# Kernel optimization log

Measured on AMD Instinct MI355X. Metric: run time of the kernel, lower is better.

## Reference

```python
import jax, jax.numpy as jnp
import numpy as np
from math import factorial

H = W = 1024
NSC = 4   # n_scales
NOR = 4   # n_orientations
NA = 9


def _grids(h, w):
    # normalized frequency grids, DC at (h//2, w//2) after fftshift
    x = (jnp.arange(w) - w // 2) / (w / 2)
    y = (jnp.arange(h) - h // 2) / (h / 2)
    xr, yr = jnp.meshgrid(x, y, indexing='xy')  # (h, w)
    ang = jnp.arctan2(yr, xr)
    rad = jnp.sqrt(xr * xr + yr * yr)
    rad = rad.at[h // 2, w // 2].set(rad[h // 2, w // 2 - 1])  # avoid log2(0)
    return jnp.log2(rad), ang


def _rc(lr, shift):
    # raised-cosine transition of width 1 (in log2 radius); returns (hi, lo) masks
    t = jnp.clip(lr + shift, 0.0, 1.0)
    return jnp.sin(0.5 * jnp.pi * t), jnp.cos(0.5 * jnp.pi * t)


def _build_pyr(im):
    """Complex steerable pyramid in the frequency domain (downsampled),
    returning (residual highpass, oriented complex bands, residual lowpass,
    unoriented bandpass per scale)."""
    h, w = im.shape
    lr, _ = _grids(h, w)
    hi0m, lo0m = _rc(lr, 1.0)
    imdft = jnp.fft.fftshift(jnp.fft.fft2(im))
    hi0 = jnp.fft.ifft2(jnp.fft.ifftshift(imdft * hi0m)).real
    lodft = imdft * lo0m
    order = NOR - 1
    const = (2.0 ** (2 * order)) * (factorial(order) ** 2) / (NOR * factorial(2 * order))
    bands, unor = [], []
    for s in range(NSC):
        hh, ww = lodft.shape
        lr, ang = _grids(hh, ww)
        him, _ = _rc(lr, 2.0)
        for b in range(NOR):
            th = ang - jnp.pi * b / NOR
            thw = jnp.mod(th + jnp.pi, 2.0 * jnp.pi) - jnp.pi
            am = 2.0 * np.sqrt(const) * (jnp.cos(th) ** order) * (jnp.abs(thw) < jnp.pi / 2)
            bdft = ((-1j) ** order) * lodft * (am * him)
            bands.append(jnp.fft.ifft2(jnp.fft.ifftshift(bdft)))
        unor.append(jnp.fft.ifft2(jnp.fft.ifftshift(lodft * him)).real)
        # downsample lowpass by 2 (crop center of spectrum), apply next lo mask
        lodft = lodft[hh // 4: hh - hh // 4, ww // 4: ww - ww // 4]
        lr2, _ = _grids(hh // 2, ww // 2)
        _, lom = _rc(lr2, 1.0)
        lodft = lodft * lom
    lowpass = jnp.fft.ifft2(jnp.fft.ifftshift(lodft)).real
    return hi0, bands, lowpass, unor


def _autocorr_crop(x, denom, le):
    F = jnp.fft.fft2(x)
    ac = jnp.fft.fftshift(jnp.fft.ifft2(F * jnp.conj(F)).real) / denom
    cx, cy = x.shape[0] // 2, x.shape[1] // 2
    return ac[cx - le: cx + le + 1, cy - le: cy + le + 1]


def _expand(t, f):
    # frequency-domain upsampling by factor f (zero-pad centered spectrum)
    mx, my = t.shape
    T = (f * f) * jnp.fft.fftshift(jnp.fft.fft2(t))
    Te = jnp.zeros((f * mx, f * my), dtype=T.dtype)
    cx, cy = f * mx // 2, f * my // 2
    Te = Te.at[cx - mx // 2: cx + mx // 2, cy - my // 2: cy + my // 2].set(T)
    return jnp.fft.ifft2(jnp.fft.ifftshift(Te))


def _ps_stats(im0):
    S, O, Na = NSC, NOR, NA
    n = im0.size
    mn0, mx0 = jnp.min(im0), jnp.max(im0)
    mean0 = jnp.mean(im0)
    var0 = jnp.sum((im0 - mean0) ** 2) / (n - 1)  # unbiased, like torch.var
    skew0 = jnp.mean((im0 - mean0) ** 3) / var0 ** 1.5
    kurt0 = jnp.mean(jnp.abs(im0 - mean0) ** 4) / var0 ** 2
    statg0 = jnp.stack([mean0, var0, skew0, kurt0, mn0, mx0])

    hi0, bands, lowpass, unor = _build_pyr(im0)
    lowpass = lowpass - jnp.mean(lowpass)
    pyr = [hi0] + bands + [lowpass]
    apyr = [jnp.abs(c) for c in pyr]
    magMeans = jnp.stack([jnp.mean(a) for a in apyr])
    apyr = [a - magMeans[i] for i, a in enumerate(apyr)]

    la = (Na - 1) // 2
    acr = jnp.zeros((Na, Na, S + 1), jnp.float32)
    ace = jnp.zeros((Na, Na, S, O), jnp.float32)
    skew0p = jnp.zeros((S + 1,), jnp.float32)
    kurt0p = jnp.zeros((S + 1,), jnp.float32)

    # ---- lowpass residual: re-filter with height-0 pyramid lowpass (lo0 mask) ----
    ch = lowpass
    le = min(min(ch.shape) // 2 - 1, la)
    lr, _ = _grids(ch.shape[0], ch.shape[1])
    _, lo0m = _rc(lr, 1.0)
    imlp = jnp.fft.ifft2(jnp.fft.ifftshift(jnp.fft.fftshift(jnp.fft.fft2(ch)) * lo0m)).real
    ac = _autocorr_crop(imlp, ch.size, le)
    acr = acr.at[la - le: la + le + 1, la - le: la + le + 1, S].set(ac)
    vari = ac[le, le]
    ok = vari / var0 > 1e-6
    skew0p = skew0p.at[S].set(jnp.where(ok, jnp.mean(imlp ** 3) / vari ** 1.5, 0.0))
    kurt0p = kurt0p.at[S].set(jnp.where(ok, jnp.mean(imlp ** 4) / vari ** 2, 3.0))

    # ---- per-band magnitude autocorr + unoriented band moments ----
    for s in range(S):
        le = la
        for b in range(O):
            chb = apyr[s * O + b + 1]
            le = min(min(chb.shape) // 2 - 1, la)
            ac = _autocorr_crop(chb, chb.size, le)
            ace = ace.at[la - le: la + le + 1, la - le: la + le + 1, s, b].set(ac)
        chu = unor[s]
        # torch stacks (real, zeros): numel doubles, cubic/quartic means halve
        ac = _autocorr_crop(chu, 2 * chu.size, le)
        acr = acr.at[la - le: la + le + 1, la - le: la + le + 1, s].set(ac)
        vari = ac[le, le]
        ok = vari / var0 > 1e-6
        skew0p = skew0p.at[s].set(jnp.where(ok, 0.5 * jnp.mean(chu ** 3) / vari ** 1.5, 0.0))
        kurt0p = kurt0p.at[s].set(jnp.where(ok, 0.5 * jnp.mean(chu ** 4) / vari ** 2, 3.0))

    # ---- cross-orientation / cross-scale correlations ----
    C0 = jnp.zeros((O, O, S + 1), jnp.float32)
    Cx0 = jnp.zeros((O, O, S), jnp.float32)
    Cr0 = jnp.zeros((2 * O, 2 * O, S + 1), jnp.float32)
    Crx0 = jnp.zeros((2 * O, 2 * O, S), jnp.float32)
    for s in range(S):
        csz = pyr[s * O + 1].size
        if s < S - 1:
            pc, rc = [], []
            for b in range(O):
                tmp = _expand(pyr[(s + 1) * O + b + 1], 2) / 4
                r, i = tmp.real, tmp.imag
                mag = jnp.sqrt(r * r + i * i)
                ph = 2.0 * jnp.arctan2(r, i)  # swapped args: faithful to source
                rc.append((mag * jnp.cos(ph), mag * jnp.sin(ph)))
                pc.append(mag)  # |(rt2, it2)| == mag
            parents = jnp.stack([(m - m.mean()).T.ravel() for m in pc], 1)
            rparents = jnp.stack([r.T.ravel() for r, _ in rc] + [i.T.ravel() for _, i in rc], 1)
        else:
            tmp = _expand(lowpass, 2).real / 4
            rparents = jnp.stack([
                tmp.ravel(),
                jnp.roll(tmp, (0, 1), (0, 1)).ravel(),
                jnp.roll(tmp, (0, -1), (0, 1)).ravel(),
                jnp.roll(tmp, (1, 0), (0, 1)).ravel(),
                jnp.roll(tmp, (-1, 0), (0, 1)).ravel()], 1)
            parents = None
        cous = jnp.stack([apyr[s * O + b + 1].T.ravel() for b in range(O)], 1)
        C0 = C0.at[:, :, s].set(cous.T @ cous / csz)
        if parents is not None:
            Cx0 = Cx0.at[:, :, s].set(cous.T @ parents / csz)
        rcous = jnp.stack([pyr[s * O + b + 1].real.T.ravel() for b in range(O)], 1)
        Cr0 = Cr0.at[:O, :O, s].set(rcous.T @ rcous / csz)
        nrp = rparents.shape[1]
        Crx0 = Crx0.at[:O, :nrp, s].set(rcous.T @ rparents / csz)
        if s == S - 1:
            Cr0 = Cr0.at[:nrp, :nrp, S].set(rparents.T @ rparents / (csz / 4))

    vHPR0 = jnp.mean(hi0 ** 2)
    return jnp.concatenate([
        statg0, magMeans, ace.ravel(), skew0p, kurt0p, acr.ravel(),
        C0.ravel(), Cx0.ravel(), Cr0.ravel(), Crx0.ravel(), vHPR0[None]])


def setup_inputs() -> dict:
    key = jax.random.key(0)
    im0 = jax.random.normal(key, (H, W), dtype=jnp.float32)
    return {"im0": im0}


def reference(im0):
    return _ps_stats(im0)
```

## Files before the change

### kernel.cpp

```cpp
#include <hip/hip_runtime.h>

#define PI_F     3.14159265358979323846f
#define TWOPI_F  6.28318530717958647692f
#define HPI_F    1.57079632679489661923f

constexpr int fftT(int N){ return N>=512 ? 256 : (N/2 < 64 ? 64 : N/2); }

#define SL_ACE 340
#define SL_ACR 996
#define SL_ALP 1160
#define SL_TOT 1280
#define REP 8

__device__ __forceinline__ float fcoord(int k, int n){
  int s = k ^ (n>>1);
  return (float)(s - (n>>1)) / (float)(n>>1);
}
__device__ __forceinline__ float lograd(int kr, int kc, int n){
  if (kr==0 && kc==0) return log2f(2.0f/(float)n);
  float x = fcoord(kc,n), y = fcoord(kr,n);
  return 0.5f*log2f(x*x+y*y);
}
__device__ __forceinline__ float rc_sin(float lr, float shift){
  float t = fminf(fmaxf(lr+shift,0.f),1.f); return __sinf(HPI_F*t);
}
__device__ __forceinline__ float rc_cos(float lr, float shift){
  float t = fminf(fmaxf(lr+shift,0.f),1.f); return __cosf(HPI_F*t);
}
__device__ __forceinline__ float cumlo(float lr, int s){
  float cl = rc_cos(lr, 1.f);
  for (int m=1;m<=s;m++) cl *= rc_cos(lr, 1.f-(float)m);
  return cl;
}
__device__ __forceinline__ float bandmask(int kr, int kc, int n, int b){
  float x = fcoord(kc,n), y = fcoord(kr,n);
  float ang = atan2f(y,x);
  float lr = lograd(kr,kc,n);
  float him = rc_sin(lr,2.0f);
  float th = ang - 0.25f*PI_F*(float)b;
  float u = th + PI_F;
  u -= TWOPI_F*floorf(u*(1.0f/TWOPI_F));
  float thw = u - PI_F;
  float c = __cosf(th);
  float am = (fabsf(thw) < HPI_F) ? (1.7888543819998317f*c*c*c) : 0.0f;
  return am*him;
}
__device__ __forceinline__ int lagIdx(int di, int dj){
  if (dj < 0 || (dj==0 && di<0)){ di=-di; dj=-dj; }
  return dj==0 ? 36+di : (dj-1)*9 + (di+4);
}
__device__ __forceinline__ void atomAddD(double* p, double v){
  unsafeAtomicAdd(p, v);
}
template<int NS>
__device__ __forceinline__ void blockAccumN(double* base, const float* vals, float* red){
  const int lane = threadIdx.x & 63, wid = threadIdx.x >> 6;
  const int nw = (int)(blockDim.x >> 6);
  #pragma unroll
  for (int k=0;k<NS;k++){
    float v = vals[k];
    #pragma unroll
    for (int o=32;o>0;o>>=1) v += __shfl_down(v,o);
    if (lane==0) red[k*nw+wid]=v;
  }
  __syncthreads();
  const int rep = (int)((blockIdx.x ^ (blockIdx.y<<1) ^ (blockIdx.z<<2)) & 7) * SL_TOT;
  if ((int)threadIdx.x < NS){
    float s=0.f;
    for (int w2=0;w2<nw;w2++) s += red[(int)threadIdx.x*nw+w2];
    atomAddD(base+rep+(int)threadIdx.x,(double)s);
  }
  __syncthreads();
}

struct ImgD { const float2* src; float2* dst; double* slots; int pre, post, b, ss; float scale; };
struct BArgs { ImgD img[6]; const float* rsrc; const float2* F; const float2* aux; float dirsign; };

#define TWI(k) ((k)+((k)>>4))

template<int N>
__global__ __launch_bounds__(fftT(N)) void k_fftB(BArgs a){
  constexpr int T = fftT(N);
  constexpr int LG = (N==1024)?10:(N==512)?9:(N==256)?8:(N==128)?7:6;
  __shared__ float2 sm[2][N];
  __shared__ float2 tw[N/2 + N/32];
  __shared__ float red[13*4];
  const ImgD d = a.img[blockIdx.y];
  const int row = blockIdx.x, tid = threadIdx.x;
  bool zrow=false;

  for (int k=tid;k<N/2;k+=T){
    float sn,cs; __sincosf(TWOPI_F*(float)k/(float)N,&sn,&cs);
    tw[TWI(k)]=make_float2(cs,sn);
  }

  switch(d.pre){
    case 0: {
      const float2* sp = d.src + (size_t)row*N;
      for (int i=tid;i<N;i+=T) sm[0][i]=sp[i];
    } break;
    case 1: {
      const float* rp = a.rsrc + (size_t)row*N;
      for (int i=tid;i<N;i+=T) sm[0][i]=make_float2(rp[i],0.f);
    } break;
    case 2: {
      const int KC = row + ((row < N/2)? 0 : (1024-N));
      const float2* Fr = a.F + (size_t)KC*1024;
      for (int i=tid;i<N;i+=T){
        int KR = i + ((i < N/2)? 0 : (1024-N));
        float2 v = Fr[KR];
        float lr = lograd(i,row,N);
        float m = cumlo(lr,d.ss)*bandmask(i,row,N,d.b);
        sm[0][i]=make_float2(-v.y*m, v.x*m);
      }
    } break;
    case 3: {
      const int KC = row + ((row < N/2)? 0 : (1024-N));
      const float2* Fr = a.F + (size_t)KC*1024;
      for (int i=tid;i<N;i+=T){
        int KR = i + ((i < N/2)? 0 : (1024-N));
        float2 v = Fr[KR];
        float lr = lograd(i,row,N);
        float m = cumlo(lr,d.ss)*rc_sin(lr,2.f);
        sm[0][i]=make_float2(v.x*m, v.y*m);
      }
    } break;
    case 4: {
      const float2* Fr = a.F + (size_t)row*1024;
      for (int i=tid;i<N;i+=T){
        float2 v = Fr[i];
        float m = rc_sin(lograd(i,row,N),1.f);
        sm[0][i]=make_float2(v.x*m, v.y*m);
      }
    } break;
    case 5: case 6: {
      constexpr int M=N/2, Q=N/4;
      const int fi = (row<Q)? row : (row>=N-Q ? row-M : -1);
      if (fi<0){
        for (int i=tid;i<N;i+=T) sm[0][i]=make_float2(0.f,0.f);
        zrow=true;
      } else {
        const int KC = fi + ((fi < M/2)? 0 : (1024-M));
        const float2* Fr = a.F + (size_t)KC*1024;
        for (int i=tid;i<N;i+=T){
          int fj = (i<Q)? i : (i>=N-Q ? i-M : -1);
          float2 r = make_float2(0.f,0.f);
          if (fj>=0){
            int KR = fj + ((fj < M/2)? 0 : (1024-M));
            float2 v = Fr[KR];
            float lr = lograd(fj,fi,M);
            if (d.pre==5){
              float m = cumlo(lr,d.ss+1)*bandmask(fj,fi,M,d.b);
              r = make_float2(-v.y*m, v.x*m);
            } else {
              if (!(fi==0 && fj==0)){
                float m = cumlo(lr,4);
                r = make_float2(v.x*m, v.y*m);
              }
            }
          }
          sm[0][i]=r;
        }
      }
    } break;
  }

  int cur=0;
  if (!zrow){
    const float ds = a.dirsign;
    int ls2 = 0;
    for (; ls2+2<=LG; ls2+=2){
      const int Ns = 1<<ls2;
      __syncthreads();
      for (int j=tid; j<N/4; j+=T){
        const int m = j & (Ns-1);
        const int base = ((j>>ls2)<<(ls2+2)) + m;
        float2 x0 = sm[cur][j];
        float2 x1 = sm[cur][j+N/4];
        float2 x2 = sm[cur][j+N/2];
        float2 x3 = sm[cur][j+3*(N/4)];
        float2 w = tw[TWI(m<<(LG-2-ls2))];
        float w1x=w.x, w1y=ds*w.y;
        float w2x = w1x*w1x - w1y*w1y, w2y = 2.f*w1x*w1y;
        float w3x = w2x*w1x - w2y*w1y, w3y = w2x*w1y + w2y*w1x;
        float2 b = make_float2(x1.x*w1x - x1.y*w1y, x1.x*w1y + x1.y*w1x);
        float2 c = make_float2(x2.x*w2x - x2.y*w2y, x2.x*w2y + x2.y*w2x);
        float2 e = make_float2(x3.x*w3x - x3.y*w3y, x3.x*w3y + x3.y*w3x);
        float t0x=x0.x+c.x, t0y=x0.y+c.y;
        float t1x=x0.x-c.x, t1y=x0.y-c.y;
        float t2x=b.x+e.x,  t2y=b.y+e.y;
        float t3x=b.x-e.x,  t3y=b.y-e.y;
        float rtx=-ds*t3y,  rty=ds*t3x;
        sm[cur^1][base]          = make_float2(t0x+t2x, t0y+t2y);
        sm[cur^1][base+Ns]       = make_float2(t1x+rtx, t1y+rty);
        sm[cur^1][base+2*Ns]     = make_float2(t0x-t2x, t0y-t2y);
        sm[cur^1][base+3*Ns]     = make_float2(t1x-rtx, t1y-rty);
      }
      cur ^= 1;
    }
    if (LG & 1){
      const int ls = LG-1, Ns = 1<<ls;
      __syncthreads();
      for (int j=tid; j<N/2; j+=T){
        const int m = j & (Ns-1);
        const int base = ((j>>ls)<<(ls+1)) + m;
        float2 va = sm[cur][j];
        float2 vb = sm[cur][j+N/2];
        float2 w = tw[TWI(m)];
        float wy = ds*w.y;
        float2 bw = make_float2(vb.x*w.x - vb.y*wy, vb.x*wy + vb.y*w.x);
        sm[cur^1][base]    = make_float2(va.x+bw.x, va.y+bw.y);
        sm[cur^1][base+Ns] = make_float2(va.x-bw.x, va.y-bw.y);
      }
      cur ^= 1;
    }
  }
  __syncthreads();

  const float sc = d.scale;
  switch(d.post){
    case 0: {
      float2* dp = d.dst + (size_t)row*N;
      for (int i=tid;i<N;i+=T){ float2 v=sm[cur][i]; dp[i]=make_float2(v.x*sc,v.y*sc); }
    } break;
    case 1: {
      float a1=0.f,a2=0.f;
      for (int i=tid;i<N;i+=T){ float v=sm[cur][i].x*sc; a1+=fabsf(v); a2+=v*v; }
      float vals[2]={a1,a2};
      blockAccumN<2>(d.slots, vals, red);
    } break;
    case 2: {
      float2* dp = d.dst + (size_t)row*N;
      float am=0.f;
      for (int i=tid;i<N;i+=T){
        float2 v=sm[cur][i]; v.x*=sc; v.y*=sc;
        float m = sqrtf(v.x*v.x+v.y*v.y);
        dp[i]=make_float2(v.x, m);
        am += m;
      }
      float vals[1]={am};
      blockAccumN<1>(d.slots, vals, red);
    } break;
    case 3: {
      float2* dp = d.dst + (size_t)row*N;
      float s2=0.f,s3=0.f,s4=0.f;
      for (int i=tid;i<N;i+=T){
        float2 v=sm[cur][i]; v.x*=sc; v.y*=sc; dp[i]=v;
        float x=v.x, x2=x*x; s2+=x2; s3+=x2*x; s4+=x2*x2;
      }
      float vals[3]={s2,s3,s4};
      blockAccumN<3>(d.slots, vals, red);
    } break;
    case 4: {
      const float2* B = a.aux;
      constexpr size_t N2 = (size_t)N*N;
      float acc[13];
      #pragma unroll
      for (int k=0;k<13;k++) acc[k]=0.f;
      for (int i=tid;i<N;i+=T){
        float2 p=sm[cur][i]; p.x*=sc; p.y*=sc;
        float m = sqrtf(p.x*p.x+p.y*p.y);
        float rp=0.f, ip=0.f;
        if (m>0.f){ rp=(p.y*p.y-p.x*p.x)/m; ip=2.f*p.x*p.y/m; }
        size_t pos = (size_t)row*N + i;
        acc[0]+=m;
        #pragma unroll
        for (int k=0;k<4;k++){
          float2 z = B[k*N2+pos];
          acc[1+k]+=z.y*m; acc[5+k]+=z.x*rp; acc[9+k]+=z.x*ip;
        }
      }
      blockAccumN<13>(d.slots, acc, red);
    } break;
  }
}

struct TArgs { float2* base[6]; int n; };
__global__ void k_trip(TArgs t){
  int bi = blockIdx.x, bj = blockIdx.y;
  if (bj < bi) return;
  const int n = t.n;
  float2* img = t.base[blockIdx.z];
  __shared__ float2 t0[32][33], t1[32][33];
  int r0=bi*32, c0=bj*32;
  for (int dy=threadIdx.y; dy<32; dy+=8){
    t0[dy][threadIdx.x] = img[(size_t)(r0+dy)*n + c0 + threadIdx.x];
    if (bi!=bj) t1[dy][threadIdx.x] = img[(size_t)(c0+dy)*n + r0 + threadIdx.x];
  }
  __syncthreads();
  for (int dy=threadIdx.y; dy<32; dy+=8){
    img[(size_t)(c0+dy)*n + r0 + threadIdx.x] = t0[threadIdx.x][dy];
    if (bi!=bj) img[(size_t)(r0+dy)*n + c0 + threadIdx.x] = t1[threadIdx.x][dy];
  }
}

struct AArgs { const float2* base[5]; double* slots[5]; int n, lgn, nmag; };
__global__ __launch_bounds__(256) void k_ac(AArgs a){
  __shared__ float t[72][73];
  __shared__ float red[41*4];
  const int z = blockIdx.z;
  const float2* img = a.base[z];
  const bool mag = z < a.nmag;
  const int n = a.n, lgn = a.lgn;
  const int ty0 = blockIdx.y*64, tx0 = blockIdx.x*64;
  for (int idx = threadIdx.x; idx < 72*72; idx += 256){
    int ly = idx/72, lx = idx-ly*72;
    int gy = (ty0 + ly - 4) & (n-1), gx = (tx0 + lx - 4) & (n-1);
    float2 v = img[((size_t)gy<<lgn) + gx];
    t[ly][lx] = mag ? v.y : v.x;
  }
  __syncthreads();
  float acc[41];
  #pragma unroll
  for (int k=0;k<41;k++) acc[k]=0.f;
  for (int p = threadIdx.x; p < 4096; p += 256){
    int ly = (p>>6) + 4, lx = (p&63) + 4;
    float m0 = t[ly][lx];
    #pragma unroll
    for (int dj=1; dj<=4; dj++)
      #pragma unroll
      for (int di=-4; di<=4; di++)
        acc[(dj-1)*9 + di+4] += m0 * t[ly+di][lx+dj];
    #pragma unroll
    for (int di=0; di<=4; di++)
      acc[36+di] += m0 * t[ly+di][lx];
  }
  blockAccumN<41>(a.slots[z], acc, red);
}

__global__ void k_init(double* S, float* out, int nout){
  int i = blockIdx.x*blockDim.x + threadIdx.x;
  if (i < REP*SL_TOT) S[i]=0.0;
  if (i < nout) out[i]=0.f;
}
__global__ __launch_bounds__(256) void k_imgstats(const float4* __restrict__ x, float* PB){
  float s1=0.f,s2=0.f,s3=0.f,s4=0.f, mn=3.4e38f, mx=-3.4e38f;
  const int base = blockIdx.x*1024 + threadIdx.x;
  #pragma unroll
  for (int it=0; it<4; ++it){
    float4 v = x[base + it*256];
    float vs[4]={v.x,v.y,v.z,v.w};
    #pragma unroll
    for (int k=0;k<4;k++){
      float t=vs[k], t2=t*t;
      s1+=t; s2+=t2; s3+=t2*t; s4+=t2*t2;
      mn=fminf(mn,t); mx=fmaxf(mx,t);
    }
  }
  __shared__ float wr[6][4];
  int lane=threadIdx.x&63, wid=threadIdx.x>>6;
  float sums[4]={s1,s2,s3,s4};
  #pragma unroll
  for (int k=0;k<4;k++){
    float v=sums[k];
    for (int o=32;o>0;o>>=1) v+=__shfl_down(v,o);
    if (lane==0) wr[k][wid]=v;
  }
  { float v=mn; for (int o=32;o>0;o>>=1) v=fminf(v,__shfl_down(v,o)); if(lane==0) wr[4][wid]=v; }
  { float v=mx; for (int o=32;o>0;o>>=1) v=fmaxf(v,__shfl_down(v,o)); if(lane==0) wr[5][wid]=v; }
  __syncthreads();
  if (threadIdx.x<4)  PB[blockIdx.x*8+threadIdx.x] = wr[threadIdx.x][0]+wr[threadIdx.x][1]+wr[threadIdx.x][2]+wr[threadIdx.x][3];
  if (threadIdx.x==4) PB[blockIdx.x*8+4] = fminf(fminf(wr[4][0],wr[4][1]),fminf(wr[4][2],wr[4][3]));
  if (threadIdx.x==5) PB[blockIdx.x*8+5] = fmaxf(fmaxf(wr[5][0],wr[5][1]),fmaxf(wr[5][2],wr[5][3]));
}
__global__ void k_gram(const float2* __restrict__ B, int n2, double* slots){
  float p[20];
  #pragma unroll
  for (int i=0;i<20;i++) p[i]=0.f;
  int stride = gridDim.x*blockDim.x;
  for (int i=blockIdx.x*blockDim.x+threadIdx.x; i<n2; i+=stride){
    float2 z0=B[i], z1=B[i+(size_t)n2], z2=B[i+2*(size_t)n2], z3=B[i+3*(size_t)n2];
    float m0=z0.y, m1=z1.y, m2=z2.y, m3=z3.y;
    float r0=z0.x, r1=z1.x, r2=z2.x, r3=z3.x;
    p[0]+=m0*m0; p[1]+=m0*m1; p[2]+=m0*m2; p[3]+=m0*m3;
    p[4]+=m1*m1; p[5]+=m1*m2; p[6]+=m1*m3;
    p[7]+=m2*m2; p[8]+=m2*m3; p[9]+=m3*m3;
    p[10]+=r0*r0; p[11]+=r0*r1; p[12]+=r0*r2; p[13]+=r0*r3;
    p[14]+=r1*r1; p[15]+=r1*r2; p[16]+=r1*r3;
    p[17]+=r2*r2; p[18]+=r2*r3; p[19]+=r3*r3;
  }
  __shared__ float red[20*4];
  blockAccumN<20>(slots,p,red);
}
__global__ void k_crx3(const float2* __restrict__ RP, const float2* __restrict__ B3, double* S){
  float a[35];
  #pragma unroll
  for (int i=0;i<35;i++) a[i]=0.f;
  int stride = gridDim.x*blockDim.x;
  for (int idx=blockIdx.x*blockDim.x+threadIdx.x; idx<16384; idx+=stride){
    int u=idx>>7, v=idx&127;
    float P0=RP[idx].x;
    float P1=RP[(u<<7) | ((v-1)&127)].x;
    float P2=RP[(u<<7) | ((v+1)&127)].x;
    float P3=RP[(((u-1)&127)<<7) | v].x;
    float P4=RP[(((u+1)&127)<<7) | v].x;
    float P[5]={P0,P1,P2,P3,P4};
    float R[4];
    #pragma unroll
    for (int b=0;b<4;b++) R[b]=B3[b*16384 + (v<<7) + u].x;
    #pragma unroll
    for (int i=0;i<4;i++)
      #pragma unroll
      for (int j=0;j<5;j++) a[i*5+j]+=R[i]*P[j];
    int k=20;
    #pragma unroll
    for (int i=0;i<5;i++)
      #pragma unroll
      for (int j=i;j<5;j++){ a[k]+=P[i]*P[j]; k++; }
  }
  __shared__ float red[35*4];
  float lo[20], hi[15];
  #pragma unroll
  for (int k=0;k<20;k++) lo[k]=a[k];
  #pragma unroll
  for (int k=0;k<15;k++) hi[k]=a[20+k];
  blockAccumN<20>(S+280, lo, red);
  blockAccumN<15>(S+300, hi, red);
}

template<int LG>
__device__ void ifft2_lds(float* re, float* im, const float2* tw, int S){
  constexpr int N=1<<LG, H=N>>1;
  const int tid=threadIdx.x, T=256;
  for (int ls=LG-1; ls>=0; --ls){
    const int h=1<<ls;
    __syncthreads();
    for (int t=tid; t<N*H; t+=T){
      int r=t>>(LG-1), j=t&(H-1);
      int m=j&(h-1);
      int i0=r*S + ((j>>ls)<<(ls+1)) + m, i1=i0+h;
      float ar=re[i0], ai=im[i0], br=re[i1], bi=im[i1];
      re[i0]=ar+br; im[i0]=ai+bi;
      float dr=ar-br, di=ai-bi;
      float2 w=tw[m<<(LG-1-ls)];
      re[i1]=dr*w.x - di*w.y;
      im[i1]=dr*w.y + di*w.x;
    }
  }
  __syncthreads();
  for (int t=tid;t<N*N;t+=T){
    int r=t>>LG, j=t&(N-1);
    int jb=(int)(__brev((unsigned)j)>>(32-LG));
    if (j<jb){
      int p=r*S+j, q=r*S+jb;
      float x=re[p]; re[p]=re[q]; re[q]=x;
      x=im[p]; im[p]=im[q]; im[q]=x;
    }
  }
  for (int ls=LG-1; ls>=0; --ls){
    const int h=1<<ls;
    __syncthreads();
    for (int t=tid; t<N*H; t+=T){
      int c=t>>(LG-1), j=t&(H-1);
      int m=j&(h-1);
      int i0=(((j>>ls)<<(ls+1))+m)*S + c, i1=i0+h*S;
      float ar=re[i0], ai=im[i0], br=re[i1], bi=im[i1];
      re[i0]=ar+br; im[i0]=ai+bi;
      float dr=ar-br, di=ai-bi;
      float2 w=tw[m<<(LG-1-ls)];
      re[i1]=dr*w.x - di*w.y;
      im[i1]=dr*w.y + di*w.x;
    }
  }
  __syncthreads();
  for (int t=tid;t<N*N;t+=T){
// ... 137 lines not shown
    int s=e>>4, i=(e>>2)&3, j=e&3;
    int a2=i<j?i:j, bb=i<j?j:i;
    int p=a2*(7-a2)/2+bb;
    double n2=npix[s];
    double Si=SD[6+s*4+i], Sj=SD[6+s*4+j];
    out[1735+(i*4+j)*5+s]=(float)((SD[40+s*20+p]-Si*Sj/n2)/n2);
    out[1879+(i*8+j)*5+s]=(float)(SD[40+s*20+10+p]/n2);
  }
  for (int e=tid; e<48; e+=256){
    int s=e>>4, j=(e>>2)&3, i=e&3;
    double n2=npix[s];
    int pb=120+(s*4+j)*13;
    double Smj=SD[pb];
    double Si=SD[6+s*4+i];
    out[1815+(i*4+j)*4+s]=(float)((SD[pb+1+i]-Si*Smj/n2)/n2);
    out[2199+(i*8+j)*4+s]=(float)(SD[pb+5+i]/n2);
    out[2199+(i*8+(j+4))*4+s]=(float)(SD[pb+9+i]/n2);
  }
  for (int e=tid; e<20; e+=256){
    int i=e/5, j=e%5;
    out[2199+(i*8+j)*4+3]=(float)(SD[280+i*5+j]/16384.0);
  }
  for (int e=tid; e<25; e+=256){
    int i=e/5, j=e%5;
    int a2=i<j?i:j, bb=i<j?j:i;
    int p=a2*(9-a2)/2+bb;
    out[1879+(i*8+j)*5+4]=(float)(SD[300+p]/4096.0);
  }
  if (tid==0){
    const double N0=1048576.0;
    double sum=sh[0], s2=sh[1], s3=sh[2], s4=sh[3];
    double mean0=sum/N0;
    double var0=(s2 - sum*mean0)/(N0-1.0);
    double m3 = s3 - 3.0*mean0*s2 + 2.0*N0*mean0*mean0*mean0;
    double m4 = s4 - 4.0*mean0*s3 + 6.0*mean0*mean0*s2 - 3.0*N0*mean0*mean0*mean0*mean0;
    out[0]=(float)mean0; out[1]=(float)var0;
    out[2]=(float)((m3/N0)/(var0*sqrt(var0)));
    out[3]=(float)((m4/N0)/(var0*var0));
    out[4]=(float)sh[4]; out[5]=(float)sh[5];
    out[6]=(float)(SD[4]/N0);
    for (int s=0;s<4;s++) for (int b=0;b<4;b++) out[7+s*4+b]=(float)(SD[6+s*4+b]/npix[s]);
    out[23]=(float)(SD[23]/4096.0);
    for (int s=0;s<4;s++){
      double n2=npix[s];
      double vari=SD[24+s*3]/(2.0*n2);
      int ok=(vari/var0>1e-6);
      out[1320+s]= ok? (float)(0.5*(SD[25+s*3]/n2)/(vari*sqrt(vari))) : 0.f;
      out[1325+s]= ok? (float)(0.5*(SD[26+s*3]/n2)/(vari*vari)) : 3.f;
    }
    { double vari=SD[36]/4096.0; int ok=(vari/var0>1e-6);
      out[1324]= ok? (float)((SD[37]/4096.0)/(vari*sqrt(vari))) : 0.f;
      out[1329]= ok? (float)((SD[38]/4096.0)/(vari*vari)) : 3.f; }
    out[2455]=(float)(SD[5]/N0);
  }
}

static void launchB(int n, int nimg, const BArgs& a, hipStream_t st){
  switch(n){
    case 1024: k_fftB<1024><<<dim3(1024,nimg),fftT(1024),0,st>>>(a); break;
    case 512:  k_fftB<512 ><<<dim3(512 ,nimg),fftT(512 ),0,st>>>(a); break;
    case 256:  k_fftB<256 ><<<dim3(256 ,nimg),fftT(256 ),0,st>>>(a); break;
    case 128:  k_fftB<128 ><<<dim3(128 ,nimg),fftT(128 ),0,st>>>(a); break;
  }
}

extern "C" void kernel_launch(void* const* d_in, const int* in_sizes, int n_in,
                              void* d_out, int out_size, void* d_ws, size_t ws_size,
                              hipStream_t stream){
  const float* im = (const float*)d_in[0];
  float* out = (float*)d_out;
  char* w = (char*)d_ws;
  float2* F   = (float2*)w;
  float2* CA4 = (float2*)(w + ((size_t)8<<20));
  float2* CC  = (float2*)(w + ((size_t)40<<20));
  float2* CB4 = (float2*)(w + ((size_t)48<<20));
  size_t off = (size_t)64<<20;
  double* S = (double*)(w+off);
  float* PB = (float*)(w+off+(size_t)REP*SL_TOT*8);

  k_init<<<40,256,0,stream>>>(S,out,2456);
  k_imgstats<<<256,256,0,stream>>>((const float4*)im,PB);

  { BArgs a{}; a.rsrc=im; a.dirsign=-1.f;
    a.img[0]=ImgD{nullptr,F,nullptr,1,0,0,0,1.f};
    launchB(1024,1,a,stream); }
  { TArgs t{}; t.base[0]=F; t.n=1024;
    k_trip<<<dim3(32,32,1),dim3(32,8),0,stream>>>(t); }
  { BArgs a{}; a.dirsign=-1.f;
    a.img[0]=ImgD{F,F,nullptr,0,0,0,0,1.f};
    launchB(1024,1,a,stream); }

  for (int s=0;s<4;s++){
    const int n=1024>>s, nt=n/32, n2=n*n, lg=10-s;
    const float inv=1.f/(float)n;
    const int nimg = (s==0)? 6 : 5;
    { BArgs a{}; a.F=F; a.dirsign=1.f;
      for (int b=0;b<4;b++) a.img[b]=ImgD{nullptr,CA4+(size_t)b*n2,nullptr,2,0,b,s,inv};
      a.img[4]=ImgD{nullptr,CC,nullptr,3,0,0,s,inv};
      if (s==0) a.img[5]=ImgD{nullptr,CB4,nullptr,4,0,0,0,inv};
      launchB(n,nimg,a,stream); }
    { TArgs t{}; t.n=n;
      for (int b=0;b<4;b++) t.base[b]=CA4+(size_t)b*n2;
      t.base[4]=CC; if (s==0) t.base[5]=CB4;
      k_trip<<<dim3(nt,nt,nimg),dim3(32,8),0,stream>>>(t); }
    { BArgs a{}; a.dirsign=1.f;
      for (int b=0;b<4;b++) a.img[b]=ImgD{CA4+(size_t)b*n2,CA4+(size_t)b*n2,S+6+s*4+b,0,2,0,0,inv};
      a.img[4]=ImgD{CC,CC,S+24+s*3,0,3,0,0,inv};
      if (s==0) a.img[5]=ImgD{CB4,nullptr,S+4,0,1,0,0,inv};
      launchB(n,nimg,a,stream); }
    k_gram<<<256,256,0,stream>>>(CA4,n2,S+40+s*20);
    { AArgs aa{}; aa.n=n; aa.lgn=lg; aa.nmag=4;
      for (int b=0;b<4;b++){ aa.base[b]=CA4+(size_t)b*n2; aa.slots[b]=S+SL_ACE+(size_t)(s*4+b)*41; }
      aa.base[4]=CC; aa.slots[4]=S+SL_ACR+(size_t)s*41;
      k_ac<<<dim3(n/64,n/64,5),256,0,stream>>>(aa); }
    if (s<3){
      const int nb = (s==0)? 2 : 4;
      for (int b0=0;b0<4;b0+=nb){
        { BArgs a{}; a.F=F; a.dirsign=1.f;
          for (int i=0;i<nb;i++) a.img[i]=ImgD{nullptr,CB4+(size_t)i*n2,nullptr,5,0,b0+i,s,inv};
          launchB(n,nb,a,stream); }
        { TArgs t{}; t.n=n;
          for (int i=0;i<nb;i++) t.base[i]=CB4+(size_t)i*n2;
          k_trip<<<dim3(nt,nt,nb),dim3(32,8),0,stream>>>(t); }
        { BArgs a{}; a.dirsign=1.f; a.aux=CA4;
          for (int i=0;i<nb;i++) a.img[i]=ImgD{CB4+(size_t)i*n2,nullptr,S+120+(size_t)(s*4+b0+i)*13,0,4,0,0,inv};
          launchB(n,nb,a,stream); }
      }
    } else {
      k_tail64<<<1,256,0,stream>>>(F,S);
      { BArgs a{}; a.F=F; a.dirsign=1.f;
        a.img[0]=ImgD{nullptr,CB4,nullptr,6,0,0,4,1.f/128.f};
        launchB(128,1,a,stream); }
      { TArgs t{}; t.base[0]=CB4; t.n=128;
        k_trip<<<dim3(4,4,1),dim3(32,8),0,stream>>>(t); }
      { BArgs a{}; a.dirsign=1.f;
        a.img[0]=ImgD{CB4,CB4,nullptr,0,0,0,0,1.f/128.f};
        launchB(128,1,a,stream); }
      k_crx3<<<64,256,0,stream>>>(CB4,CA4,S);
    }
  }
  k_final<<<1,256,0,stream>>>(S,PB,out);
  (void)in_sizes; (void)n_in; (void)out_size; (void)ws_size;
}
```

Before: 489.8 us.

## Batch oriented band FFTs per block, fold gram into autocorr kernel, vectorize lags

The oriented-band row FFTs now load each spectrum row once into registers, with the radial mask and angle precomputed, and loop over all bands inside one block. This replaces one block per band and removes the repeated global loads and atan2/log work. The separate gram kernel is merged into k_ac as an extra z-slice, saving a launch. The autocorrelation inner loop is reorganised so each thread handles two adjacent columns with float2 shared loads. Because one block now runs several bands in sequence, the band FFT launches have fewer blocks and less parallelism.

```diff
diff --git a/kernel.cpp b/kernel.cpp
--- a/kernel.cpp
+++ b/kernel.cpp
@@ -32,18 +32,13 @@
   for (int m=1;m<=s;m++) cl *= rc_cos(lr, 1.f-(float)m);
   return cl;
 }
-__device__ __forceinline__ float bandmask(int kr, int kc, int n, int b){
-  float x = fcoord(kc,n), y = fcoord(kr,n);
-  float ang = atan2f(y,x);
-  float lr = lograd(kr,kc,n);
-  float him = rc_sin(lr,2.0f);
+__device__ __forceinline__ float bandang(float ang, int b){
   float th = ang - 0.25f*PI_F*(float)b;
   float u = th + PI_F;
   u -= TWOPI_F*floorf(u*(1.0f/TWOPI_F));
   float thw = u - PI_F;
   float c = __cosf(th);
-  float am = (fabsf(thw) < HPI_F) ? (1.7888543819998317f*c*c*c) : 0.0f;
-  return am*him;
+  return (fabsf(thw) < HPI_F) ? (1.7888543819998317f*c*c*c) : 0.0f;
 }
 __device__ __forceinline__ int lagIdx(int di, int dj){
   if (dj < 0 || (dj==0 && di<0)){ di=-di; dj=-dj; }
@@ -73,7 +68,7 @@
   __syncthreads();
 }
 
-struct ImgD { const float2* src; float2* dst; double* slots; int pre, post, b, ss; float scale; };
+struct ImgD { const float2* src; float2* dst; double* slots; int pre, post, b, ss; float scale; int nb; };
 struct BArgs { ImgD img[6]; const float* rsrc; const float2* F; const float2* aux; float dirsign; };
 
 #define TWI(k) ((k)+((k)>>4))
@@ -82,6 +77,7 @@
 __global__ __launch_bounds__(fftT(N)) void k_fftB(BArgs a){
   constexpr int T = fftT(N);
   constexpr int LG = (N==1024)?10:(N==512)?9:(N==256)?8:(N==128)?7:6;
+  constexpr int NE = N/T;
   __shared__ float2 sm[2][N];
   __shared__ float2 tw[N/2 + N/32];
   __shared__ float red[13*4];
@@ -94,184 +90,219 @@
     tw[TWI(k)]=make_float2(cs,sn);
   }
 
-  switch(d.pre){
-    case 0: {
-      const float2* sp = d.src + (size_t)row*N;
-      for (int i=tid;i<N;i+=T) sm[0][i]=sp[i];
-    } break;
-    case 1: {
-      const float* rp = a.rsrc + (size_t)row*N;
-      for (int i=tid;i<N;i+=T) sm[0][i]=make_float2(rp[i],0.f);
-    } break;
-    case 2: {
-      const int KC = row + ((row < N/2)? 0 : (1024-N));
+  const int NB = (d.pre==7 || d.pre==8) ? d.nb : 1;
+  float2 vv[NE]; float lrm[NE]; float angv[NE];
+
+  if (d.pre==7){
+    const int KC = row + ((row < N/2)? 0 : (1024-N));
+    const float2* Fr = a.F + (size_t)KC*1024;
+    #pragma unroll
+    for (int e=0;e<NE;e++){
+      int i = tid + e*T;
+      int KR = i + ((i < N/2)? 0 : (1024-N));
+      float2 v = Fr[KR];
+      float lr = lograd(i,row,N);
+      lrm[e] = cumlo(lr,d.ss)*rc_sin(lr,2.f);
+      angv[e] = atan2f(fcoord(i,N), fcoord(row,N));
+      vv[e] = make_float2(-v.y, v.x);
+    }
+  } else if (d.pre==8){
+    constexpr int M=N/2, Q=N/4;
+    const int fi = (row<Q)? row : (row>=N-Q ? row-M : -1);
+    if (fi<0) zrow=true;
+    else {
+      const int KC = fi + ((fi < M/2)? 0 : (1024-M));
       const float2* Fr = a.F + (size_t)KC*1024;
-      for (int i=tid;i<N;i+=T){
-        int KR = i + ((i < N/2)? 0 : (1024-N));
-        float2 v = Fr[KR];
-        float lr = lograd(i,row,N);
-        float m = cumlo(lr,d.ss)*bandmask(i,row,N,d.b);
-        sm[0][i]=make_float2(-v.y*m, v.x*m);
+      #pragma unroll
+      for (int e=0;e<NE;e++){
+        int i = tid + e*T;
+        int fj = (i<Q)? i : (i>=N-Q ? i-M : -1);
+        if (fj<0){ lrm[e]=0.f; angv[e]=0.f; vv[e]=make_float2(0.f,0.f); }
+        else {
+          int KR = fj + ((fj < M/2)? 0 : (1024-M));
+          float2 v = Fr[KR];
+          float lr = lograd(fj,fi,M);
+          lrm[e] = cumlo(lr,d.ss+1)*rc_sin(lr,2.f);
+          angv[e] = atan2f(fcoord(fj,M), fcoord(fi,M));
+          vv[e] = make_float2(-v.y, v.x);
+        }
       }
-    } break;
-    case 3: {
-      const int KC = row + ((row < N/2)? 0 : (1024-N));
-      const float2* Fr = a.F + (size_t)KC*1024;
-      for (int i=tid;i<N;i+=T){
-        int KR = i + ((i < N/2)? 0 : (1024-N));
-        float2 v = Fr[KR];
-        float lr = lograd(i,row,N);
-        float m = cumlo(lr,d.ss)*rc_sin(lr,2.f);
-        sm[0][i]=make_float2(v.x*m, v.y*m);
+    }
+  }
+
+  for (int bi=0; bi<NB; ++bi){
+    __syncthreads();
+    if (d.pre==7 || d.pre==8){
+      if (!zrow){
+        #pragma unroll
+        for (int e=0;e<NE;e++){
+          int i = tid + e*T;
+          float m = lrm[e]*bandang(angv[e], d.b+bi);
+          sm[0][i]=make_float2(vv[e].x*m, vv[e].y*m);
+        }
+      } else if (bi==0){
+        for (int i=tid;i<N;i+=T) sm[0][i]=make_float2(0.f,0.f);
       }
-    } break;
-    case 4: {
-      const float2* Fr = a.F + (size_t)row*1024;
-      for (int i=tid;i<N;i+=T){
-        float2 v = Fr[i];
-        float m = rc_sin(lograd(i,row,N),1.f);
-        sm[0][i]=make_float2(v.x*m, v.y*m);
-      }
-    } break;
-    case 5: case 6: {
-      constexpr int M=N/2, Q=N/4;
-      const int fi = (row<Q)? row : (row>=N-Q ? row-M : -1);
-      if (fi<0){
-        for (int i=tid;i<N;i+=T) sm[0][i]=make_float2(0.f,0.f);
-        zrow=true;
-      } else {
-        const int KC = fi + ((fi < M/2)? 0 : (1024-M));
+    } else switch(d.pre){
+      case 0: {
+        const float2* sp = d.src + (size_t)row*N;
+        for (int i=tid;i<N;i+=T) sm[0][i]=sp[i];
+      } break;
+      case 1: {
+        const float* rp = a.rsrc + (size_t)row*N;
+        for (int i=tid;i<N;i+=T) sm[0][i]=make_float2(rp[i],0.f);
+      } break;
+      case 3: {
+        const int KC = row + ((row < N/2)? 0 : (1024-N));
         const float2* Fr = a.F + (size_t)KC*1024;
         for (int i=tid;i<N;i+=T){
-          int fj = (i<Q)? i : (i>=N-Q ? i-M : -1);
-          float2 r = make_float2(0.f,0.f);
-          if (fj>=0){
-            int KR = fj + ((fj < M/2)? 0 : (1024-M));
-            float2 v = Fr[KR];
-            float lr = lograd(fj,fi,M);
-            if (d.pre==5){
-              float m = cumlo(lr,d.ss+1)*bandmask(fj,fi,M,d.b);
-              r = make_float2(-v.y*m, v.x*m);
-            } else {
-              if (!(fi==0 && fj==0)){
-                float m = cumlo(lr,4);
-                r = make_float2(v.x*m, v.y*m);
-              }
+          int KR = i + ((i < N/2)? 0 : (1024-N));
+          float2 v = Fr[KR];
+          float lr = lograd(i,row,N);
+          float m = cumlo(lr,d.ss)*rc_sin(lr,2.f);
+          sm[0][i]=make_float2(v.x*m, v.y*m);
+        }
+      } break;
+      case 4: {
+        const float2* Fr = a.F + (size_t)row*1024;
+        for (int i=tid;i<N;i+=T){
+          float2 v = Fr[i];
+          float m = rc_sin(lograd(i,row,N),1.f);
+          sm[0][i]=make_float2(v.x*m, v.y*m);
+        }
+      } break;
+      case 6: {
+        constexpr int M=N/2, Q=N/4;
+        const int fi = (row<Q)? row : (row>=N-Q ? row-M : -1);
+        if (fi<0){
+          for (int i=tid;i<N;i+=T) sm[0][i]=make_float2(0.f,0.f);
+          zrow=true;
+        } else {
+          const int KC = fi + ((fi < M/2)? 0 : (1024-M));
+          const float2* Fr = a.F + (size_t)KC*1024;
+          for (int i=tid;i<N;i+=T){
+            int fj = (i<Q)? i : (i>=N-Q ? i-M : -1);
+            float2 r = make_float2(0.f,0.f);
+            if (fj>=0 && !(fi==0 && fj==0)){
+              int KR = fj + ((fj < M/2)? 0 : (1024-M));
+              float2 v = Fr[KR];
+              float m = cumlo(lograd(fj,fi,M),4);
+              r = make_float2(v.x*m, v.y*m);
             }
+            sm[0][i]=r;
           }
-          sm[0][i]=r;
-        }
+        }
+      } break;
+    }
+
+    int cur=0;
+    if (!zrow){
+      const float ds = a.dirsign;
+      int ls2 = 0;
+      for (; ls2+2<=LG; ls2+=2){
+        const int Ns = 1<<ls2;
+        __syncthreads();
+        for (int j=tid; j<N/4; j+=T){
+          const int m = j & (Ns-1);
+          const int base = ((j>>ls2)<<(ls2+2)) + m;
+          float2 x0 = sm[cur][j];
+          float2 x1 = sm[cur][j+N/4];
+          float2 x2 = sm[cur][j+N/2];
+          float2 x3 = sm[cur][j+3*(N/4)];
+          float2 w = tw[TWI(m<<(LG-2-ls2))];
+          float w1x=w.x, w1y=ds*w.y;
+          float w2x = w1x*w1x - w1y*w1y, w2y = 2.f*w1x*w1y;
+          float w3x = w2x*w1x - w2y*w1y, w3y = w2x*w1y + w2y*w1x;
+          float2 b = make_float2(x1.x*w1x - x1.y*w1y, x1.x*w1y + x1.y*w1x);
+          float2 c = make_float2(x2.x*w2x - x2.y*w2y, x2.x*w2y + x2.y*w2x);
+          float2 e = make_float2(x3.x*w3x - x3.y*w3y, x3.x*w3y + x3.y*w3x);
+          float t0x=x0.x+c.x, t0y=x0.y+c.y;
+          float t1x=x0.x-c.x, t1y=x0.y-c.y;
+          float t2x=b.x+e.x,  t2y=b.y+e.y;
+          float t3x=b.x-e.x,  t3y=b.y-e.y;
+          float rtx=-ds*t3y,  rty=ds*t3x;
+          sm[cur^1][base]          = make_float2(t0x+t2x, t0y+t2y);
+          sm[cur^1][base+Ns]       = make_float2(t1x+rtx, t1y+rty);
+          sm[cur^1][base+2*Ns]     = make_float2(t0x-t2x, t0y-t2y);
+          sm[cur^1][base+3*Ns]     = make_float2(t1x-rtx, t1y-rty);
+        }
+        cur ^= 1;
       }
-    } break;
-  }
-
-  int cur=0;
-  if (!zrow){
-    const float ds = a.dirsign;
-    int ls2 = 0;
-    for (; ls2+2<=LG; ls2+=2){
-      const int Ns = 1<<ls2;
-      __syncthreads();
-      for (int j=tid; j<N/4; j+=T){
-        const int m = j & (Ns-1);
-        const int base = ((j>>ls2)<<(ls2+2)) + m;
-        float2 x0 = sm[cur][j];
-        float2 x1 = sm[cur][j+N/4];
-        float2 x2 = sm[cur][j+N/2];
-        float2 x3 = sm[cur][j+3*(N/4)];
-        float2 w = tw[TWI(m<<(LG-2-ls2))];
-        float w1x=w.x, w1y=ds*w.y;
-        float w2x = w1x*w1x - w1y*w1y, w2y = 2.f*w1x*w1y;
-        float w3x = w2x*w1x - w2y*w1y, w3y = w2x*w1y + w2y*w1x;
-        float2 b = make_float2(x1.x*w1x - x1.y*w1y, x1.x*w1y + x1.y*w1x);
-        float2 c = make_float2(x2.x*w2x - x2.y*w2y, x2.x*w2y + x2.y*w2x);
-        float2 e = make_float2(x3.x*w3x - x3.y*w3y, x3.x*w3y + x3.y*w3x);
-        float t0x=x0.x+c.x, t0y=x0.y+c.y;
-        float t1x=x0.x-c.x, t1y=x0.y-c.y;
-        float t2x=b.x+e.x,  t2y=b.y+e.y;
-        float t3x=b.x-e.x,  t3y=b.y-e.y;
-        float rtx=-ds*t3y,  rty=ds*t3x;
-        sm[cur^1][base]          = make_float2(t0x+t2x, t0y+t2y);
-        sm[cur^1][base+Ns]       = make_float2(t1x+rtx, t1y+rty);
-        sm[cur^1][base+2*Ns]     = make_float2(t0x-t2x, t0y-t2y);
-        sm[cur^1][base+3*Ns]     = make_float2(t1x-rtx, t1y-rty);
+      if (LG & 1){
+        const int ls = LG-1, Ns = 1<<ls;
+        __syncthreads();
+        for (int j=tid; j<N/2; j+=T){
+          const int m = j & (Ns-1);
+          const int base = ((j>>ls)<<(ls+1)) + m;
+          float2 va = sm[cur][j];
+          float2 vb = sm[cur][j+N/2];
+          float2 w = tw[TWI(m)];
+          float wy = ds*w.y;
+          float2 bw = make_float2(vb.x*w.x - vb.y*wy, vb.x*wy + vb.y*w.x);
+          sm[cur^1][base]    = make_float2(va.x+bw.x, va.y+bw.y);
+          sm[cur^1][base+Ns] = make_float2(va.x-bw.x, va.y-bw.y);
+        }
+        cur ^= 1;
       }
-      cur ^= 1;
-    }
-    if (LG & 1){
-      const int ls = LG-1, Ns = 1<<ls;
-      __syncthreads();
-      for (int j=tid; j<N/2; j+=T){
-        const int m = j & (Ns-1);
-        const int base = ((j>>ls)<<(ls+1)) + m;
-        float2 va = sm[cur][j];
-        float2 vb = sm[cur][j+N/2];
-        float2 w = tw[TWI(m)];
-        float wy = ds*w.y;
-        float2 bw = make_float2(vb.x*w.x - vb.y*wy, vb.x*wy + vb.y*w.x);
-        sm[cur^1][base]    = make_float2(va.x+bw.x, va.y+bw.y);
-        sm[cur^1][base+Ns] = make_float2(va.x-bw.x, va.y-bw.y);
-      }
-      cur ^= 1;
-    }
-  }
-  __syncthreads();
-
-  const float sc = d.scale;
-  switch(d.post){
-    case 0: {
-      float2* dp = d.dst + (size_t)row*N;
-      for (int i=tid;i<N;i+=T){ float2 v=sm[cur][i]; dp[i]=make_float2(v.x*sc,v.y*sc); }
-    } break;
-    case 1: {
-      float a1=0.f,a2=0.f;
-      for (int i=tid;i<N;i+=T){ float v=sm[cur][i].x*sc; a1+=fabsf(v); a2+=v*v; }
-      float vals[2]={a1,a2};
-      blockAccumN<2>(d.slots, vals, red);
-    } break;
-    case 2: {
-      float2* dp = d.dst + (size_t)row*N;
-      float am=0.f;
-      for (int i=tid;i<N;i+=T){
-        float2 v=sm[cur][i]; v.x*=sc; v.y*=sc;
-        float m = sqrtf(v.x*v.x+v.y*v.y);
-        dp[i]=make_float2(v.x, m);
-        am += m;
-      }
-      float vals[1]={am};
-      blockAccumN<1>(d.slots, vals, red);
-    } break;
-    case 3: {
-      float2* dp = d.dst + (size_t)row*N;
-      float s2=0.f,s3=0.f,s4=0.f;
-      for (int i=tid;i<N;i+=T){
-        float2 v=sm[cur][i]; v.x*=sc; v.y*=sc; dp[i]=v;
-        float x=v.x, x2=x*x; s2+=x2; s3+=x2*x; s4+=x2*x2;
-      }
-      float vals[3]={s2,s3,s4};
-      blockAccumN<3>(d.slots, vals, red);
-    } break;
-    case 4: {
-      const float2* B = a.aux;
-      constexpr size_t N2 = (size_t)N*N;
-      float acc[13];
-      #pragma unroll
-      for (int k=0;k<13;k++) acc[k]=0.f;
-      for (int i=tid;i<N;i+=T){
-        float2 p=sm[cur][i]; p.x*=sc; p.y*=sc;
-        float m = sqrtf(p.x*p.x+p.y*p.y);
-        float rp=0.f, ip=0.f;
-        if (m>0.f){ rp=(p.y*p.y-p.x*p.x)/m; ip=2.f*p.x*p.y/m; }
-        size_t pos = (size_t)row*N + i;
-        acc[0]+=m;
+    }
+    __syncthreads();
+
+    const float sc = d.scale;
+    switch(d.post){
+      case 0: {
+        float2* dp = d.dst + (size_t)bi*N*N + (size_t)row*N;
+        for (int i=tid;i<N;i+=T){ float2 v=sm[cur][i]; dp[i]=make_float2(v.x*sc,v.y*sc); }
+      } break;
+      case 1: {
+        float a1=0.f,a2=0.f;
+        for (int i=tid;i<N;i+=T){ float v=sm[cur][i].x*sc; a1+=fabsf(v); a2+=v*v; }
+        float vals[2]={a1,a2};
+        blockAccumN<2>(d.slots, vals, red);
+      } break;
+      case 2: {
+        float2* dp = d.dst + (size_t)row*N;
+        float am=0.f;
+        for (int i=tid;i<N;i+=T){
+          float2 v=sm[cur][i]; v.x*=sc; v.y*=sc;
+          float m = sqrtf(v.x*v.x+v.y*v.y);
+          dp[i]=make_float2(v.x, m);
+          am += m;
+        }
+        float vals[1]={am};
+        blockAccumN<1>(d.slots, vals, red);
+      } break;
+      case 3: {
+        float2* dp = d.dst + (size_t)row*N;
+        float s2=0.f,s3=0.f,s4=0.f;
+        for (int i=tid;i<N;i+=T){
+          float2 v=sm[cur][i]; v.x*=sc; v.y*=sc; dp[i]=v;
+          float x=v.x, x2=x*x; s2+=x2; s3+=x2*x; s4+=x2*x2;
+        }
+        float vals[3]={s2,s3,s4};
+        blockAccumN<3>(d.slots, vals, red);
+      } break;
+      case 4: {
+        const float2* B = a.aux;
+        constexpr size_t N2 = (size_t)N*N;
+        float acc[13];
         #pragma unroll
-        for (int k=0;k<4;k++){
-          float2 z = B[k*N2+pos];
-          acc[1+k]+=z.y*m; acc[5+k]+=z.x*rp; acc[9+k]+=z.x*ip;
-        }
-      }
-      blockAccumN<13>(d.slots, acc, red);
-    } break;
+        for (int k=0;k<13;k++) acc[k]=0.f;
+        for (int i=tid;i<N;i+=T){
+          float2 p=sm[cur][i]; p.x*=sc; p.y*=sc;
+          float m = sqrtf(p.x*p.x+p.y*p.y);
+          float rp=0.f, ip=0.f;
+          if (m>0.f){ rp=(p.y*p.y-p.x*p.x)/m; ip=2.f*p.x*p.y/m; }
+          size_t pos = (size_t)row*N + i;
+          acc[0]+=m;
+          #pragma unroll
+          for (int k=0;k<4;k++){
+            float2 z = B[k*N2+pos];
+            acc[1+k]+=z.y*m; acc[5+k]+=z.x*rp; acc[9+k]+=z.x*ip;
+          }
+        }
+        blockAccumN<13>(d.slots, acc, red);
+      } break;
+    }
   }
 }
 
@@ -294,14 +325,37 @@
   }
 }
 
-struct AArgs { const float2* base[5]; double* slots[5]; int n, lgn, nmag; };
+struct AArgs { const float2* base[6]; double* slots[6]; int n, lgn, nmag; };
 __global__ __launch_bounds__(256) void k_ac(AArgs a){
-  __shared__ float t[72][73];
   __shared__ float red[41*4];
+  __shared__ __align__(16) float t[72][74];
   const int z = blockIdx.z;
+  const int n = a.n;
+  if (z==5){
+    const float2* B = a.base[5];
+    const size_t n2 = (size_t)n*n;
+    float p[20];
+    #pragma unroll
+    for (int i=0;i<20;i++) p[i]=0.f;
+    const size_t nbk = (size_t)gridDim.x*gridDim.y;
+    const size_t bid = (size_t)blockIdx.y*gridDim.x + blockIdx.x;
+    for (size_t i = bid*256 + threadIdx.x; i<n2; i += nbk*256){
+      float2 z0=B[i], z1=B[i+n2], z2=B[i+2*n2], z3=B[i+3*n2];
+      float m0=z0.y, m1=z1.y, m2=z2.y, m3=z3.y;
+      float r0=z0.x, r1=z1.x, r2=z2.x, r3=z3.x;
+      p[0]+=m0*m0; p[1]+=m0*m1; p[2]+=m0*m2; p[3]+=m0*m3;
+      p[4]+=m1*m1; p[5]+=m1*m2; p[6]+=m1*m3;
+      p[7]+=m2*m2; p[8]+=m2*m3; p[9]+=m3*m3;
+      p[10]+=r0*r0; p[11]+=r0*r1; p[12]+=r0*r2; p[13]+=r0*r3;
+      p[14]+=r1*r1; p[15]+=r1*r2; p[16]+=r1*r3;
+      p[17]+=r2*r2; p[18]+=r2*r3; p[19]+=r3*r3;
+    }
+    blockAccumN<20>(a.slots[5], p, red);
+    return;
+  }
   const float2* img = a.base[z];
   const bool mag = z < a.nmag;
-  const int n = a.n, lgn = a.lgn;
+  const int lgn = a.lgn;
   const int ty0 = blockIdx.y*64, tx0 = blockIdx.x*64;
   for (int idx = threadIdx.x; idx < 72*72; idx += 256){
     int ly = idx/72, lx = idx-ly*72;
@@ -313,17 +367,26 @@
   float acc[41];
   #pragma unroll
   for (int k=0;k<41;k++) acc[k]=0.f;
-  for (int p = threadIdx.x; p < 4096; p += 256){
-    int ly = (p>>6) + 4, lx = (p&63) + 4;
-    float m0 = t[ly][lx];
-    #pragma unroll
-    for (int dj=1; dj<=4; dj++)
-      #pragma unroll
-      for (int di=-4; di<=4; di++)
-        acc[(dj-1)*9 + di+4] += m0 * t[ly+di][lx+dj];
-    #pragma unroll
-    for (int di=0; di<=4; di++)
-      acc[36+di] += m0 * t[ly+di][lx];
+  const int c  = threadIdx.x & 31;
+  const int rg = threadIdx.x >> 5;
+  const int x0 = 4 + 2*c;
+  #pragma unroll
+  for (int k=0;k<8;k++){
+    const int y = 4 + rg + 8*k;
+    const float2 c2 = *(const float2*)&t[y][x0];
+    #pragma unroll
+    for (int di=-4; di<=4; ++di){
+      const float* rp = &t[y+di][x0];
+      const float2 ra  = *(const float2*)rp;
+      const float2 rb  = *(const float2*)(rp+2);
+      const float2 rc2 = *(const float2*)(rp+4);
+      const float r0=ra.x, r1=ra.y, r2=rb.x, r3=rb.y, r4=rc2.x, r5=rc2.y;
+      if (di>=0) acc[36+di] += c2.x*r0 + c2.y*r1;
+      acc[di+4]      += c2.x*r1 + c2.y*r2;
+      acc[9+di+4]    += c2.x*r2 + c2.y*r3;
+      acc[18+di+4]   += c2.x*r3 + c2.y*r4;
+      acc[27+di+4]   += c2.x*r4 + c2.y*r5;
+    }
   }
   blockAccumN<41>(a.slots[z], acc, red);
 }
@@ -362,25 +425,6 @@
   if (threadIdx.x<4)  PB[blockIdx.x*8+threadIdx.x] = wr[threadIdx.x][0]+wr[threadIdx.x][1]+wr[threadIdx.x][2]+wr[threadIdx.x][3];
   if (threadIdx.x==4) PB[blockIdx.x*8+4] = fminf(fminf(wr[4][0],wr[4][1]),fminf(wr[4][2],wr[4][3]));
   if (threadIdx.x==5) PB[blockIdx.x*8+5] = fmaxf(fmaxf(wr[5][0],wr[5][1]),fmaxf(wr[5][2],wr[5][3]));
-}
-__global__ void k_gram(const float2* __restrict__ B, int n2, double* slots){
-  float p[20];
-  #pragma unroll
-  for (int i=0;i<20;i++) p[i]=0.f;
-  int stride = gridDim.x*blockDim.x;
-  for (int i=blockIdx.x*blockDim.x+threadIdx.x; i<n2; i+=stride){
-    float2 z0=B[i], z1=B[i+(size_t)n2], z2=B[i+2*(size_t)n2], z3=B[i+3*(size_t)n2];
-    float m0=z0.y, m1=z1.y, m2=z2.y, m3=z3.y;
-    float r0=z0.x, r1=z1.x, r2=z2.x, r3=z3.x;
-    p[0]+=m0*m0; p[1]+=m0*m1; p[2]+=m0*m2; p[3]+=m0*m3;
-    p[4]+=m1*m1; p[5]+=m1*m2; p[6]+=m1*m3;
-    p[7]+=m2*m2; p[8]+=m2*m3; p[9]+=m3*m3;
-    p[10]+=r0*r0; p[11]+=r0*r1; p[12]+=r0*r2; p[13]+=r0*r3;
-    p[14]+=r1*r1; p[15]+=r1*r2; p[16]+=r1*r3;
-    p[17]+=r2*r2; p[18]+=r2*r3; p[19]+=r3*r3;
-  }
-  __shared__ float red[20*4];
-  blockAccumN<20>(slots,p,red);
 }
 __global__ void k_crx3(const float2* __restrict__ RP, const float2* __restrict__ B3, double* S){
   float a[35];
@@ -684,59 +728,58 @@
   k_imgstats<<<256,256,0,stream>>>((const float4*)im,PB);
 
   { BArgs a{}; a.rsrc=im; a.dirsign=-1.f;
-    a.img[0]=ImgD{nullptr,F,nullptr,1,0,0,0,1.f};
+    a.img[0]=ImgD{nullptr,F,nullptr,1,0,0,0,1.f,1};
     launchB(1024,1,a,stream); }
   { TArgs t{}; t.base[0]=F; t.n=1024;
     k_trip<<<dim3(32,32,1),dim3(32,8),0,stream>>>(t); }
   { BArgs a{}; a.dirsign=-1.f;
-    a.img[0]=ImgD{F,F,nullptr,0,0,0,0,1.f};
+    a.img[0]=ImgD{F,F,nullptr,0,0,0,0,1.f,1};
     launchB(1024,1,a,stream); }
 
   for (int s=0;s<4;s++){
     const int n=1024>>s, nt=n/32, n2=n*n, lg=10-s;
     const float inv=1.f/(float)n;
-    const int nimg = (s==0)? 6 : 5;
     { BArgs a{}; a.F=F; a.dirsign=1.f;
-      for (int b=0;b<4;b++) a.img[b]=ImgD{nullptr,CA4+(size_t)b*n2,nullptr,2,0,b,s,inv};
-      a.img[4]=ImgD{nullptr,CC,nullptr,3,0,0,s,inv};
-      if (s==0) a.img[5]=ImgD{nullptr,CB4,nullptr,4,0,0,0,inv};
-      launchB(n,nimg,a,stream); }
+      a.img[0]=ImgD{nullptr,CA4,nullptr,7,0,0,s,inv,4};
+      a.img[1]=ImgD{nullptr,CC,nullptr,3,0,0,s,inv,1};
+      if (s==0) a.img[2]=ImgD{nullptr,CB4,nullptr,4,0,0,0,inv,1};
+      launchB(n,(s==0)?3:2,a,stream); }
     { TArgs t{}; t.n=n;
       for (int b=0;b<4;b++) t.base[b]=CA4+(size_t)b*n2;
       t.base[4]=CC; if (s==0) t.base[5]=CB4;
-      k_trip<<<dim3(nt,nt,nimg),dim3(32,8),0,stream>>>(t); }
+      k_trip<<<dim3(nt,nt,(s==0)?6:5),dim3(32,8),0,stream>>>(t); }
     { BArgs a{}; a.dirsign=1.f;
-      for (int b=0;b<4;b++) a.img[b]=ImgD{CA4+(size_t)b*n2,CA4+(size_t)b*n2,S+6+s*4+b,0,2,0,0,inv};
-      a.img[4]=ImgD{CC,CC,S+24+s*3,0,3,0,0,inv};
-      if (s==0) a.img[5]=ImgD{CB4,nullptr,S+4,0,1,0,0,inv};
-      launchB(n,nimg,a,stream); }
-    k_gram<<<256,256,0,stream>>>(CA4,n2,S+40+s*20);
+      for (int b=0;b<4;b++) a.img[b]=ImgD{CA4+(size_t)b*n2,CA4+(size_t)b*n2,S+6+s*4+b,0,2,0,0,inv,1};
+      a.img[4]=ImgD{CC,CC,S+24+s*3,0,3,0,0,inv,1};
+      if (s==0) a.img[5]=ImgD{CB4,nullptr,S+4,0,1,0,0,inv,1};
+      launchB(n,(s==0)?6:5,a,stream); }
     { AArgs aa{}; aa.n=n; aa.lgn=lg; aa.nmag=4;
       for (int b=0;b<4;b++){ aa.base[b]=CA4+(size_t)b*n2; aa.slots[b]=S+SL_ACE+(size_t)(s*4+b)*41; }
       aa.base[4]=CC; aa.slots[4]=S+SL_ACR+(size_t)s*41;
-      k_ac<<<dim3(n/64,n/64,5),256,0,stream>>>(aa); }
+      aa.base[5]=CA4; aa.slots[5]=S+40+(size_t)s*20;
+      k_ac<<<dim3(n/64,n/64,6),256,0,stream>>>(aa); }
     if (s<3){
       const int nb = (s==0)? 2 : 4;
       for (int b0=0;b0<4;b0+=nb){
         { BArgs a{}; a.F=F; a.dirsign=1.f;
-          for (int i=0;i<nb;i++) a.img[i]=ImgD{nullptr,CB4+(size_t)i*n2,nullptr,5,0,b0+i,s,inv};
-          launchB(n,nb,a,stream); }
+          a.img[0]=ImgD{nullptr,CB4,nullptr,8,0,b0,s,inv,nb};
+          launchB(n,1,a,stream); }
         { TArgs t{}; t.n=n;
           for (int i=0;i<nb;i++) t.base[i]=CB4+(size_t)i*n2;
           k_trip<<<dim3(nt,nt,nb),dim3(32,8),0,stream>>>(t); }
         { BArgs a{}; a.dirsign=1.f; a.aux=CA4;
-          for (int i=0;i<nb;i++) a.img[i]=ImgD{CB4+(size_t)i*n2,nullptr,S+120+(size_t)(s*4+b0+i)*13,0,4,0,0,inv};
+          for (int i=0;i<nb;i++) a.img[i]=ImgD{CB4+(size_t)i*n2,nullptr,S+120+(size_t)(s*4+b0+i)*13,0,4,0,0,inv,1};
           launchB(n,nb,a,stream); }
       }
     } else {
       k_tail64<<<1,256,0,stream>>>(F,S);
       { BArgs a{}; a.F=F; a.dirsign=1.f;
-        a.img[0]=ImgD{nullptr,CB4,nullptr,6,0,0,4,1.f/128.f};
+        a.img[0]=ImgD{nullptr,CB4,nullptr,6,0,0,4,1.f/128.f,1};
         launchB(128,1,a,stream); }
       { TArgs t{}; t.base[0]=CB4; t.n=128;
         k_trip<<<dim3(4,4,1),dim3(32,8),0,stream>>>(t); }
       { BArgs a{}; a.dirsign=1.f;
-        a.img[0]=ImgD{CB4,CB4,nullptr,0,0,0,0,1.f/128.f};
+        a.img[0]=ImgD{CB4,CB4,nullptr,0,0,0,0,1.f/128.f,1};
         launchB(128,1,a,stream); }
       k_crx3<<<64,256,0,stream>>>(CB4,CA4,S);
     }
```

After: 550.5 us. +12.4%, slower.
